# Kernel tuning notes

Hardware: AMD Instinct MI355X
Metric: run time of the kernel (lower is better)

Reference implementation:

```python
import jax, jax.numpy as jnp
import numpy as np

B, L = 2048, 2  # batch, num_layers


def ry_mat(theta):
    c = jnp.cos(theta / 2).astype(jnp.complex64)
    s = jnp.sin(theta / 2).astype(jnp.complex64)
    return jnp.stack([jnp.stack([c, -s], -1), jnp.stack([s, c], -1)], -2)


def rz_mat(theta):
    e = jnp.exp(-0.5j * theta.astype(jnp.complex64))
    z = jnp.zeros_like(e)
    return jnp.stack([jnp.stack([e, z], -1), jnp.stack([z, jnp.conj(e)], -1)], -2)


def apply_1q(state, U, wire):
    # state: (N,2,2,2,2); U: (2,2) shared or (N,2,2) per-patch
    ax = wire + 1
    s = jnp.moveaxis(state, ax, -1)
    if U.ndim == 3:
        s = jnp.einsum('n...b,nab->n...a', s, U)
    else:
        s = jnp.einsum('...b,ab->...a', s, U)
    return jnp.moveaxis(s, -1, ax)


def apply_cnot(state, c, t):
    s0 = jnp.take(state, 0, axis=c + 1)
    s1 = jnp.take(state, 1, axis=c + 1)
    tt = t + 1 if t < c else t  # target axis index after removing control axis
    return jnp.stack([s0, jnp.flip(s1, axis=tt)], axis=c + 1)


def circuit(data, weights):
    # data: (N,4) angles; weights: (L,4,2). Batched analytic 4-qubit statevector sim.
    n = data.shape[0]
    state = jnp.zeros((n, 2, 2, 2, 2), jnp.complex64).at[:, 0, 0, 0, 0].set(1.0)
    for q in range(4):
        state = apply_1q(state, ry_mat(data[:, q]), q)
    for l in range(weights.shape[0]):
        for q in range(4):
            state = apply_1q(state, ry_mat(weights[l, q, 0]), q)
            state = apply_1q(state, rz_mat(weights[l, q, 1]), q)
        state = apply_cnot(state, 0, 1)
        state = apply_cnot(state, 2, 3)
    probs = state.real ** 2 + state.imag ** 2  # (N,2,2,2,2)
    zs = [jnp.take(probs, 0, axis=q + 1).sum((1, 2, 3))
          - jnp.take(probs, 1, axis=q + 1).sum((1, 2, 3)) for q in range(4)]
    return jnp.stack(zs, -1)  # (N,4) PauliZ expvals


def setup_inputs() -> dict:
    key = jax.random.key(0)
    k1, k2, k3 = jax.random.split(key, 3)
    x = jax.random.uniform(k1, (B, 1, 28, 28), jnp.float32)
    weights = jax.random.normal(k2, (L, 4, 2), jnp.float32)
    Wc = jax.random.normal(k3, (10, 4 * 14 * 14), jnp.float32) * 0.02
    bc = jnp.zeros((10,), jnp.float32)
    return {"x": x, "weights": weights, "Wc": Wc, "bc": bc}


def reference(x, weights, Wc, bc):
    b = x.shape[0]
    # non-overlapping 2x2 patches, row-major within patch (matches torch unfold/view)
    patches = x.reshape(b, 14, 2, 14, 2).transpose(0, 1, 3, 2, 4).reshape(b * 14 * 14, 4)
    qf = circuit(patches, weights).reshape(b, -1)  # (B, 784)
    logits = qf @ Wc.T + bc
    return jax.nn.log_softmax(logits, axis=-1)
```

## Files before the change

kernel.cpp:

```cpp
#include <hip/hip_runtime.h>
#include <hip/hip_bf16.h>

__global__ __launch_bounds__(64) void setup_U_kernel(const float* __restrict__ w,
                                                     int L, float* __restrict__ U)
{
    const int j = threadIdx.x;
    if (j >= 16) return;

    float ar[16], ai[16];
#pragma unroll
    for (int k = 0; k < 16; ++k) { ar[k] = (k == j) ? 1.f : 0.f; ai[k] = 0.f; }

    for (int l = 0; l < L; ++l) {
#pragma unroll
        for (int q = 0; q < 4; ++q) {
            const float thy = w[l * 8 + q * 2 + 0];
            const float thz = w[l * 8 + q * 2 + 1];
            float cy, sy, cz, sz;
            __sincosf(0.5f * thy, &sy, &cy);
            __sincosf(0.5f * thz, &sz, &cz);
            const int st = 8 >> q;
#pragma unroll
            for (int idx = 0; idx < 16; ++idx) {
                if ((idx & st) == 0) {
                    const int i1 = idx + st;
                    const float a0r = ar[idx], a1r = ar[i1];
                    const float a0i = ai[idx], a1i = ai[i1];
                    ar[idx] = cy * a0r - sy * a1r;  ar[i1] = sy * a0r + cy * a1r;
                    ai[idx] = cy * a0i - sy * a1i;  ai[i1] = sy * a0i + cy * a1i;
                }
            }
#pragma unroll
            for (int idx = 0; idx < 16; ++idx) {
                const float r = ar[idx], im = ai[idx];
                if ((idx & st) == 0) {
                    ar[idx] = r * cz + im * sz;
                    ai[idx] = im * cz - r * sz;
                } else {
                    ar[idx] = r * cz - im * sz;
                    ai[idx] = im * cz + r * sz;
                }
            }
        }
#pragma unroll
        for (int idx = 0; idx < 16; ++idx) {
            if ((idx & 8) && !(idx & 4)) {
                const int i2 = idx | 4;
                float tr = ar[idx], ti = ai[idx];
                ar[idx] = ar[i2]; ai[idx] = ai[i2];
                ar[i2] = tr;      ai[i2] = ti;
            }
        }
#pragma unroll
        for (int idx = 0; idx < 16; ++idx) {
            if ((idx & 2) && !(idx & 1)) {
                const int i2 = idx | 1;
                float tr = ar[idx], ti = ai[idx];
                ar[idx] = ar[i2]; ai[idx] = ai[i2];
                ar[i2] = tr;      ai[i2] = ti;
            }
        }
    }

#pragma unroll
    for (int a = 0; a < 16; ++a) {
        U[a * 16 + j]       = ar[a];
        U[256 + a * 16 + j] = ai[a];
    }
}

__global__ __launch_bounds__(256) void quanv_fused_kernel(
    const float* __restrict__ x, const float* __restrict__ Wc,
    const float* __restrict__ bc, const float* __restrict__ U,
    float* __restrict__ out)
{
    const int b   = blockIdx.x;
    const int tid = threadIdx.x;

    __shared__ float qf[784];
    __shared__ float red[40];
    __shared__ float logits_s[10];

    {
        const int p  = (tid < 196) ? tid : 0;
        const int pi = p / 14, pj = p % 14;
        const float* xb = x + b * 784 + pi * 56 + pj * 2;
        const float d0 = xb[0], d1 = xb[1], d2 = xb[28], d3 = xb[29];

        float c0, s0, c1, s1, c2, s2, c3, s3;
        __sincosf(0.5f * d0, &s0, &c0);
        __sincosf(0.5f * d1, &s1, &c1);
        __sincosf(0.5f * d2, &s2, &c2);
        __sincosf(0.5f * d3, &s3, &c3);

        float psi[16];
        {
            const float w0[2] = {c0, s0}, w1[2] = {c1, s1};
            const float w2[2] = {c2, s2}, w3[2] = {c3, s3};
#pragma unroll
            for (int i0 = 0; i0 < 2; ++i0)
#pragma unroll
                for (int i1 = 0; i1 < 2; ++i1) {
                    const float ab = w0[i0] * w1[i1];
#pragma unroll
                    for (int i2 = 0; i2 < 2; ++i2) {
                        const float abc = ab * w2[i2];
#pragma unroll
                        for (int i3 = 0; i3 < 2; ++i3)
                            psi[i0 * 8 + i1 * 4 + i2 * 2 + i3] = abc * w3[i3];
                    }
                }
        }

        float z0 = 0.f, z1 = 0.f, z2 = 0.f, z3 = 0.f;
#pragma unroll
        for (int a = 0; a < 16; ++a) {
            float Ar = 0.f, Ai = 0.f;
#pragma unroll
            for (int k = 0; k < 16; ++k) {
                Ar = fmaf(U[a * 16 + k],       psi[k], Ar);
                Ai = fmaf(U[256 + a * 16 + k], psi[k], Ai);
            }
            const float pr = Ar * Ar + Ai * Ai;
            z0 += (a & 8) ? -pr : pr;
            z1 += (a & 4) ? -pr : pr;
            z2 += (a & 2) ? -pr : pr;
            z3 += (a & 1) ? -pr : pr;
        }

        if (tid < 196) {
            qf[tid * 4 + 0] = z0;
            qf[tid * 4 + 1] = z1;
            qf[tid * 4 + 2] = z2;
            qf[tid * 4 + 3] = z3;
        }
    }
    __syncthreads();

    float acc[10];
#pragma unroll
    for (int k = 0; k < 10; ++k) acc[k] = 0.f;

    for (int f = tid; f < 784; f += 256) {
        const float v = qf[f];
#pragma unroll
        for (int k = 0; k < 10; ++k)
            acc[k] = fmaf(v, Wc[k * 784 + f], acc[k]);
    }

#pragma unroll
    for (int k = 0; k < 10; ++k) {
#pragma unroll
        for (int off = 32; off > 0; off >>= 1)
            acc[k] += __shfl_down(acc[k], off, 64);
    }
    const int wave = tid >> 6;
    const int lane = tid & 63;
    if (lane == 0) {
#pragma unroll
        for (int k = 0; k < 10; ++k) red[wave * 10 + k] = acc[k];
    }
    __syncthreads();

    if (tid < 10)
        logits_s[tid] = bc[tid] + red[tid] + red[10 + tid] + red[20 + tid] + red[30 + tid];
    __syncthreads();

    if (tid < 10) {
        float m = logits_s[0];
#pragma unroll
        for (int jj = 1; jj < 10; ++jj) m = fmaxf(m, logits_s[jj]);
        float se = 0.f;
#pragma unroll
        for (int jj = 0; jj < 10; ++jj) se += __expf(logits_s[jj] - m);
        out[b * 10 + tid] = logits_s[tid] - m - __logf(se);
    }
}

extern "C" void kernel_launch(void* const* d_in, const int* in_sizes, int n_in,
                              void* d_out, int out_size, void* d_ws, size_t ws_size,
                              hipStream_t stream)
{
    const float* x  = (const float*)d_in[0];
    const float* w  = (const float*)d_in[1];
    const float* Wc = (const float*)d_in[2];
    const float* bc = (const float*)d_in[3];
    float* out = (float*)d_out;
    float* U   = (float*)d_ws;

    const int L = in_sizes[1] / 8;
    const int B = in_sizes[0] / 784;

    setup_U_kernel<<<1, 64, 0, stream>>>(w, L, U);
    quanv_fused_kernel<<<B, 256, 0, stream>>>(x, Wc, bc, U, out);
}
```

Measured before the change: 76.23 us.

## Split each patch's 16x16 unitary matvec across 16 lanes with shuffle butterfly

Each patch's product state is staged in shared memory. Groups of 16 threads then compute one output amplitude each, with that thread's U row held in registers. The four PauliZ expectations come from a Walsh-Hadamard butterfly done with xor-shuffles. This replaces the old scheme, where 196 of 256 threads each did a full 512-FMA matvec reading U from global memory, which left threads idle and serialized the work. In exchange it adds a shared-memory round trip, an extra barrier, shuffles and redundant work in the padded last iteration.

```diff
diff --git a/kernel.cpp b/kernel.cpp
--- a/kernel.cpp
+++ b/kernel.cpp
@@ -69,6 +69,9 @@
     }
 }
 
+#define NP 196
+#define PSTRIDE 20
+
 __global__ __launch_bounds__(256) void quanv_fused_kernel(
     const float* __restrict__ x, const float* __restrict__ Wc,
     const float* __restrict__ bc, const float* __restrict__ U,
@@ -76,14 +79,30 @@
 {
     const int b   = blockIdx.x;
     const int tid = threadIdx.x;
-
+    const int a   = tid & 15;
+    const int g   = tid >> 4;
+
+    __shared__ __align__(16) float psi_s[NP][PSTRIDE];
     __shared__ float qf[784];
     __shared__ float red[40];
     __shared__ float logits_s[10];
 
+    float Ur[16], Ui[16];
     {
-        const int p  = (tid < 196) ? tid : 0;
-        const int pi = p / 14, pj = p % 14;
+        const float4* U4 = (const float4*)U;
+#pragma unroll
+        for (int j = 0; j < 4; ++j) {
+            const float4 r  = U4[a * 4 + j];
+            const float4 im = U4[64 + a * 4 + j];
+            Ur[4 * j + 0] = r.x;  Ur[4 * j + 1] = r.y;
+            Ur[4 * j + 2] = r.z;  Ur[4 * j + 3] = r.w;
+            Ui[4 * j + 0] = im.x; Ui[4 * j + 1] = im.y;
+            Ui[4 * j + 2] = im.z; Ui[4 * j + 3] = im.w;
+        }
+    }
+
+    if (tid < NP) {
+        const int pi = tid / 14, pj = tid % 14;
         const float* xb = x + b * 784 + pi * 56 + pj * 2;
         const float d0 = xb[0], d1 = xb[1], d2 = xb[28], d3 = xb[29];
 
@@ -93,46 +112,68 @@
         __sincosf(0.5f * d2, &s2, &c2);
         __sincosf(0.5f * d3, &s3, &c3);
 
+        const float w0[2] = {c0, s0}, w1[2] = {c1, s1};
+        const float w2[2] = {c2, s2}, w3[2] = {c3, s3};
+        float4* dst = (float4*)&psi_s[tid][0];
+#pragma unroll
+        for (int i0 = 0; i0 < 2; ++i0)
+#pragma unroll
+            for (int i1 = 0; i1 < 2; ++i1) {
+                const float ab = w0[i0] * w1[i1];
+#pragma unroll
+                for (int i2 = 0; i2 < 2; ++i2) {
+                    const float abc = ab * w2[i2];
+                    float4 v;
+                    v.x = abc * w3[0];
+                    v.y = abc * w3[1];
+                    (void)v;
+                    psi_s[tid][i0 * 8 + i1 * 4 + i2 * 2 + 0] = abc * w3[0];
+                    psi_s[tid][i0 * 8 + i1 * 4 + i2 * 2 + 1] = abc * w3[1];
+                }
+            }
+        (void)dst;
+    }
+
+    float sgn[4];
+#pragma unroll
+    for (int s = 0; s < 4; ++s) sgn[s] = (tid & (1 << s)) ? -1.f : 1.f;
+
+    __syncthreads();
+
+#pragma unroll 1
+    for (int it = 0; it < 13; ++it) {
+        const int p  = it * 16 + g;
+        const int pc = (p < NP) ? p : (NP - 1);
+
         float psi[16];
         {
-            const float w0[2] = {c0, s0}, w1[2] = {c1, s1};
-            const float w2[2] = {c2, s2}, w3[2] = {c3, s3};
-#pragma unroll
-            for (int i0 = 0; i0 < 2; ++i0)
-#pragma unroll
-                for (int i1 = 0; i1 < 2; ++i1) {
-                    const float ab = w0[i0] * w1[i1];
-#pragma unroll
-                    for (int i2 = 0; i2 < 2; ++i2) {
-                        const float abc = ab * w2[i2];
-#pragma unroll
-                        for (int i3 = 0; i3 < 2; ++i3)
-                            psi[i0 * 8 + i1 * 4 + i2 * 2 + i3] = abc * w3[i3];
-                    }
-                }
-        }
-
-        float z0 = 0.f, z1 = 0.f, z2 = 0.f, z3 = 0.f;
-#pragma unroll
-        for (int a = 0; a < 16; ++a) {
-            float Ar = 0.f, Ai = 0.f;
-#pragma unroll
-            for (int k = 0; k < 16; ++k) {
-                Ar = fmaf(U[a * 16 + k],       psi[k], Ar);
-                Ai = fmaf(U[256 + a * 16 + k], psi[k], Ai);
-            }
-            const float pr = Ar * Ar + Ai * Ai;
-            z0 += (a & 8) ? -pr : pr;
-            z1 += (a & 4) ? -pr : pr;
-            z2 += (a & 2) ? -pr : pr;
-            z3 += (a & 1) ? -pr : pr;
-        }
-
-        if (tid < 196) {
-            qf[tid * 4 + 0] = z0;
-            qf[tid * 4 + 1] = z1;
-            qf[tid * 4 + 2] = z2;
-            qf[tid * 4 + 3] = z3;
+            const float4* prow = (const float4*)&psi_s[pc][0];
+#pragma unroll
+            for (int j = 0; j < 4; ++j) {
+                const float4 v = prow[j];
+                psi[4 * j + 0] = v.x; psi[4 * j + 1] = v.y;
+                psi[4 * j + 2] = v.z; psi[4 * j + 3] = v.w;
+            }
+        }
+
+        float Ar = 0.f, Ai = 0.f;
+#pragma unroll
+        for (int k = 0; k < 16; ++k) {
+            Ar = fmaf(Ur[k], psi[k], Ar);
+            Ai = fmaf(Ui[k], psi[k], Ai);
+        }
+        float v = Ar * Ar + Ai * Ai;
+
+#pragma unroll
+        for (int s = 0; s < 4; ++s) {
+            const float t = __shfl_xor(v, 1 << s, 64);
+            v = fmaf(sgn[s], v, t);
+        }
+        if (p < NP) {
+            if (a == 8)      qf[p * 4 + 0] = v;
+            else if (a == 4) qf[p * 4 + 1] = v;
+            else if (a == 2) qf[p * 4 + 2] = v;
+            else if (a == 1) qf[p * 4 + 3] = v;
         }
     }
     __syncthreads();
```

Measured after the change: 84.46 us. +10.8%, slower.
